# Optimization experiments

Hardware: AMD Instinct MI355X
Metric: run time of the kernel (lower is better)

## Reference

```python
import jax, jax.numpy as jnp
import numpy as np

N, NF, INF, NHID = 8192, 128, 128, 16


def _gcn(x, adj, dis, W, b):
    # GraphConvolution: support = x @ W; aggregate with distance-weighted adjacency
    support = x @ W  # [N, out]
    return (adj * dis) @ support + b


def setup_inputs() -> dict:
    key = jax.random.key(0)
    ks = jax.random.split(key, 26)

    def lin(k, i, o):
        kw, kb = jax.random.split(k)
        W = jax.random.uniform(kw, (i, o), jnp.float32, -1.0, 1.0) / np.sqrt(i).astype(np.float32)
        b = jax.random.uniform(kb, (o,), jnp.float32, -1.0, 1.0) / np.sqrt(i).astype(np.float32)
        return W, b

    x = jax.random.normal(ks[0], (N, NF), jnp.float32)
    adj = jax.random.uniform(ks[1], (N, N), jnp.float32)
    dis = jax.random.uniform(ks[2], (N, N), jnp.float32)

    W1, b1 = lin(ks[3], NF, NF)        # linear1
    Wg1, bg1 = lin(ks[4], NF, INF)     # gc1
    Wm1, bm1 = lin(ks[5], INF, 64)     # linear_med1
    Wm2, bm2 = lin(ks[6], 64, 128)     # linear_med2
    Wm3, bm3 = lin(ks[7], 128, 64)     # linear_med3
    Wm4, bm4 = lin(ks[8], 64, 64)      # linear_med4
    Wgh, bgh = lin(ks[9], 64, 64)      # gconv_hidden[0]
    W2, b2 = lin(ks[10], 64, 32)       # linear2
    Wg2, bg2 = lin(ks[11], 32, 32)     # gc2
    W3, b3 = lin(ks[12], 32, NHID)     # linear3

    return dict(x=x, adj=adj, dis=dis, W1=W1, b1=b1, Wg1=Wg1, bg1=bg1,
                Wm1=Wm1, bm1=bm1, Wm2=Wm2, bm2=bm2, Wm3=Wm3, bm3=bm3,
                Wm4=Wm4, bm4=bm4, Wgh=Wgh, bgh=bgh, W2=W2, b2=b2,
                Wg2=Wg2, bg2=bg2, W3=W3, b3=b3)


def reference(x, adj, dis, W1, b1, Wg1, bg1, Wm1, bm1, Wm2, bm2, Wm3, bm3,
              Wm4, bm4, Wgh, bgh, W2, b2, Wg2, bg2, W3, b3):
    lrelu = lambda v: jax.nn.leaky_relu(v, 0.2)
    x0 = _gcn(x @ W1 + b1, adj, dis, Wg1, bg1)
    x0 = lrelu(x0 @ Wm1 + bm1)
    x0 = lrelu(x0 @ Wm2 + bm2)
    x0 = lrelu(x0 @ Wm3 + bm3)
    x0 = jax.nn.relu(x0 @ Wm4 + bm4)
    x_res = x0
    x0 = jax.nn.relu(_gcn(x0, adj, dis, Wgh, bgh) + x_res)  # one hidden gconv layer
    x0 = x0 @ W2 + b2
    x0 = _gcn(x0, adj, dis, Wg2, bg2)
    return x0 @ W3 + b3
```

## Files before the change

### kernel.cpp

```cpp
#include <hip/hip_runtime.h>
#include <hip/hip_bf16.h>

#define NROWS 8192
typedef unsigned short u16;
typedef short bf16x8 __attribute__((ext_vector_type(8)));
typedef short bf16x4 __attribute__((ext_vector_type(4)));
typedef float f32x4 __attribute__((ext_vector_type(4)));

__device__ __forceinline__ u16 f2b(float f) {
    unsigned u = __float_as_uint(f);
    unsigned r = (u + 0x7fffu + ((u >> 16) & 1u)) >> 16;
    return (u16)r;
}
__device__ __forceinline__ float b2f(u16 v) {
    return __uint_as_float(((unsigned)v) << 16);
}

template<int MODE> __device__ __forceinline__ float actf(float v) {
    if constexpr (MODE == 1) return fmaxf(v, 0.f);
    else if constexpr (MODE == 2) return v > 0.f ? v : 0.2f * v;
    else return v;
}

__global__ __launch_bounds__(256) void fold1(
    const float* __restrict__ W1, const float* __restrict__ b1,
    const float* __restrict__ Wg1,
    const float* __restrict__ W2, const float* __restrict__ b2,
    const float* __restrict__ Wg2, float* __restrict__ ws) {
    float* T2 = ws + 9376;
    float* v1 = ws + 11424;
    float* v2 = ws + 11552;
    float* T1 = ws + 16384;
    const int tid = threadIdx.x, b = blockIdx.x;
    if (b < 16) {
        int i = b * 8 + (tid >> 5), j4 = (tid & 31) << 2;
        float4 acc = {0, 0, 0, 0};
        for (int k = 0; k < 128; ++k) {
            float a = W1[i * 128 + k];
            float4 g = *(const float4*)&Wg1[k * 128 + j4];
            acc.x += a * g.x; acc.y += a * g.y; acc.z += a * g.z; acc.w += a * g.w;
        }
        *(float4*)&T1[i * 128 + j4] = acc;
    } else if (b == 16) {
        if (tid < 128) {
            float s = 0;
            for (int k = 0; k < 128; ++k) s += b1[k] * Wg1[k * 128 + tid];
            v1[tid] = s;
        } else if (tid < 160) {
            int j = tid - 128;
            float s = 0;
            for (int k = 0; k < 32; ++k) s += b2[k] * Wg2[k * 32 + j];
            v2[j] = s;
        }
    } else {
        for (int o4 = tid; o4 < 64 * 8; o4 += 256) {
            int i = o4 >> 3, j4 = (o4 & 7) << 2;
            float4 acc = {0, 0, 0, 0};
            for (int k = 0; k < 32; ++k) {
                float a = W2[i * 32 + k];
                float4 g = *(const float4*)&Wg2[k * 32 + j4];
                acc.x += a * g.x; acc.y += a * g.y; acc.z += a * g.z; acc.w += a * g.w;
            }
            *(float4*)&T2[i * 32 + j4] = acc;
        }
    }
}

__global__ __launch_bounds__(256) void fold2(
    const float* __restrict__ Wm1, const float* __restrict__ bm1,
    const float* __restrict__ bg1,
    const float* __restrict__ W3, const float* __restrict__ b3,
    const float* __restrict__ bg2, float* __restrict__ ws) {
    float* WA = ws + 0;
    float* bA = ws + 8192;
    float* cA = ws + 8256;
    float* WB = ws + 8320;
    float* bB = ws + 9344;
    float* cB = ws + 9360;
    const float* T2 = ws + 9376;
    const float* v1 = ws + 11424;
    const float* v2 = ws + 11552;
    const float* T1 = ws + 16384;
    const int tid = threadIdx.x, b = blockIdx.x;
    if (b < 8) {
        int i = b * 16 + (tid >> 4), j4 = (tid & 15) << 2;
        float4 acc = {0, 0, 0, 0};
        for (int k = 0; k < 128; ++k) {
            float a = T1[i * 128 + k];
            float4 g = *(const float4*)&Wm1[k * 64 + j4];
            acc.x += a * g.x; acc.y += a * g.y; acc.z += a * g.z; acc.w += a * g.w;
        }
        *(float4*)&WA[i * 64 + j4] = acc;
    } else if (b == 8) {
        if (tid < 64) {
            float s = 0, c = 0;
            for (int k = 0; k < 128; ++k) {
                s += v1[k] * Wm1[k * 64 + tid];
                c += bg1[k] * Wm1[k * 64 + tid];
            }
            bA[tid] = s; cA[tid] = c + bm1[tid];
        } else if (tid < 80) {
            int j = tid - 64;
            float s = 0, c = 0;
            for (int k = 0; k < 32; ++k) {
                s += v2[k] * W3[k * 16 + j];
                c += bg2[k] * W3[k * 16 + j];
            }
            bB[j] = s; cB[j] = c + b3[j];
        }
    } else {
        int i = tid >> 2, j4 = (tid & 3) << 2;
        float4 acc = {0, 0, 0, 0};
        for (int k = 0; k < 32; ++k) {
            float a = T2[i * 32 + k];
            float4 g = *(const float4*)&W3[k * 16 + j4];
            acc.x += a * g.x; acc.y += a * g.y; acc.z += a * g.z; acc.w += a * g.w;
        }
        *(float4*)&WB[i * 16 + j4] = acc;
    }
}

template<int K, int M, int AIN, int AOUT, int OUTT>
__global__ __launch_bounds__(256) void gemm_rows(
    const float* __restrict__ in, const float* __restrict__ W,
    const float* __restrict__ bias, void* __restrict__ outv) {
    constexpr int RB = 32;
    constexpr int TNs = (M >= 64) ? 4 : 2;
    constexpr int TXs = M / TNs;
    constexpr int TYs = 256 / TXs;
    constexpr int TMs = RB / TYs;
    static_assert(TMs >= 1 && TMs * TYs == RB, "bad cfg");
    __shared__ float in_t[K][RB + 4];
    __shared__ float w_s[K * M];
    __shared__ float bias_s[M];
    const int tid = threadIdx.x;
    const int b0 = blockIdx.x * RB;
    constexpr int K4 = K / 4;
    for (int g = tid; g < RB * K4; g += 256) {
        int r = g / K4, c4 = g % K4;
        float4 v = *(const float4*)&in[(size_t)(b0 + r) * K + c4 * 4];
        v.x = actf<AIN>(v.x); v.y = actf<AIN>(v.y);
        v.z = actf<AIN>(v.z); v.w = actf<AIN>(v.w);
        in_t[c4 * 4 + 0][r] = v.x;
        in_t[c4 * 4 + 1][r] = v.y;
        in_t[c4 * 4 + 2][r] = v.z;
        in_t[c4 * 4 + 3][r] = v.w;
    }
    for (int g = tid; g < K * M / 4; g += 256)
        ((float4*)w_s)[g] = ((const float4*)W)[g];
    if (tid < M) bias_s[tid] = bias ? bias[tid] : 0.f;
    __syncthreads();

    const int tx = tid % TXs, ty = tid / TXs;
    const int c0 = tx * TNs, r0 = ty * TMs;
    float acc[TMs][TNs] = {};
    for (int k = 0; k < K; ++k) {
        float a[TMs];
#pragma unroll
        for (int m = 0; m < TMs; ++m) a[m] = in_t[k][r0 + m];
        float w[TNs];
#pragma unroll
        for (int n = 0; n < TNs; ++n) w[n] = w_s[k * M + c0 + n];
#pragma unroll
        for (int m = 0; m < TMs; ++m)
#pragma unroll
            for (int n = 0; n < TNs; ++n) acc[m][n] += a[m] * w[n];
    }
#pragma unroll
    for (int m = 0; m < TMs; ++m) {
        float vres[TNs];
#pragma unroll
        for (int n = 0; n < TNs; ++n) vres[n] = actf<AOUT>(acc[m][n] + bias_s[c0 + n]);
        if constexpr (OUTT == 0) {
            float* op = &((float*)outv)[(size_t)(b0 + r0 + m) * M + c0];
            if constexpr (TNs == 4) { float4 o4 = {vres[0], vres[1], vres[2], vres[3]}; *(float4*)op = o4; }
            else                    { float2 o2 = {vres[0], vres[1]}; *(float2*)op = o2; }
        } else {
            u16* ot = (u16*)outv;
#pragma unroll
            for (int n = 0; n < TNs; ++n)
                ot[(size_t)(c0 + n) * NROWS + (b0 + r0 + m)] = f2b(vres[n]);
        }
    }
}

template<int K, int M, int AOUT, int OMODE>
__device__ __forceinline__ void layer_step(
    const float (*pin)[17], const float* __restrict__ w,
    const float* __restrict__ bias,
    float (*pout)[17], float* __restrict__ gout, u16* __restrict__ stout,
    int b0, int tid) {
    constexpr int TXs = M / 4;
    constexpr int TYs = 256 / TXs;
    constexpr int TMs = 16 / TYs;
    static_assert(TMs >= 1, "cfg");
    const int tx = tid % TXs, ty = tid / TXs;
    const int c0 = tx * 4, r0 = ty * TMs;
    float acc[TMs][4] = {};
    for (int k = 0; k < K; ++k) {
        float4 wv = *(const float4*)&w[k * M + c0];
#pragma unroll
        for (int m = 0; m < TMs; ++m) {
            float a = pin[k][r0 + m];
            acc[m][0] += a * wv.x; acc[m][1] += a * wv.y;
            acc[m][2] += a * wv.z; acc[m][3] += a * wv.w;
        }
    }
#pragma unroll
    for (int m = 0; m < TMs; ++m) {
        float v[4];
#pragma unroll
        for (int n = 0; n < 4; ++n) {
            float bv = bias ? bias[c0 + n] : 0.f;
            v[n] = actf<AOUT>(acc[m][n] + bv);
        }
        if constexpr (OMODE != 2) {
#pragma unroll
            for (int n = 0; n < 4; ++n) pout[c0 + n][r0 + m] = v[n];
        }
        if constexpr (OMODE == 1) {
            float4 o = {v[0], v[1], v[2], v[3]};
            *(float4*)&gout[(size_t)(b0 + r0 + m) * M + c0] = o;
        }
        if constexpr (OMODE == 2) {
#pragma unroll
            for (int n = 0; n < 4; ++n)
                stout[(size_t)(c0 + n) * NROWS + (b0 + r0 + m)] = f2b(v[n]);
        }
    }
}

__global__ __launch_bounds__(256) void med_chain(
    const float* __restrict__ gA,
    const float* __restrict__ Wm2, const float* __restrict__ bm2,
    const float* __restrict__ Wm3, const float* __restrict__ bm3,
    const float* __restrict__ Wm4, const float* __restrict__ bm4,
    const float* __restrict__ Wgh,
    float* __restrict__ h4, u16* __restrict__ St) {
    __shared__ __align__(16) float P0[64][17];
    __shared__ __align__(16) float P1[128][17];
    __shared__ __align__(16) float P2[64][17];
    const int tid = threadIdx.x;
    const int b0 = blockIdx.x * 16;

    {
        int r = tid >> 4, c4 = tid & 15;
        float4 v = *(const float4*)&gA[(size_t)(b0 + r) * 64 + c4 * 4];
        P0[c4 * 4 + 0][r] = actf<2>(v.x);
        P0[c4 * 4 + 1][r] = actf<2>(v.y);
        P0[c4 * 4 + 2][r] = actf<2>(v.z);
        P0[c4 * 4 + 3][r] = actf<2>(v.w);
    }
    __syncthreads();
    layer_step<64, 128, 2, 0>(P0, Wm2, bm2, P1, nullptr, nullptr, b0, tid);
    __syncthreads();
    layer_step<128, 64, 2, 0>(P1, Wm3, bm3, P2, nullptr, nullptr, b0, tid);
    __syncthreads();
    layer_step<64, 64, 1, 1>(P2, Wm4, bm4, P0, h4, nullptr, b0, tid);
    __syncthreads();
    layer_step<64, 64, 0, 2>(P0, Wgh, nullptr, nullptr, nullptr, St, b0, tid);
}

template<int F, int MODE, int KS>
__global__ __launch_bounds__(256) void agg_mfma(
    u16* __restrict__ Abf, const float* __restrict__ adj,
    const float* __restrict__ dis, const u16* __restrict__ St,
    u16* __restrict__ Pout) {
    constexpr int CT = F / 16;
    constexpr int BK = 128;
    constexpr int KCH = NROWS / KS;
    constexpr int NCH = KCH / BK;
    __shared__ __align__(16) u16 As[64 * BK];
    __shared__ __align__(16) u16 Bs[F * BK];
    const int tid  = threadIdx.x;
    const int lane = tid & 63;
    const int wid  = tid >> 6;
    const int i0   = blockIdx.x * 64;
    const int ky   = blockIdx.y;
    const int l15  = lane & 15;
    const int kb   = (lane >> 4) * 8;
    const int k0   = ky * KCH;
    f32x4 acc[CT] = {};

    for (int ch = 0; ch < NCH; ++ch) {
        const int kc = k0 + ch * BK;
        if constexpr (MODE == 0) {
#pragma unroll
            for (int r = 0; r < (64 * BK) / (256 * 8); ++r) {
                int e8  = r * 256 + tid;
                int row = e8 >> 4;
                int col = (e8 & 15) * 8;
                bf16x8 v = *(const bf16x8*)(Abf + (size_t)(i0 + row) * NROWS + kc + col);
                int bo = ((row * BK + col) * 2) ^ ((row & 7) << 4);
                *(bf16x8*)((char*)As + bo) = v;
            }
        } else {
#pragma unroll
            for (int r = 0; r < (64 * BK) / (256 * 4); ++r) {
                int e4  = r * 256 + tid;
                int row = e4 >> 5;
                int col = (e4 & 31) * 4;
                size_t g = (size_t)(i0 + row) * NROWS + kc + col;
                f32x4 a = __builtin_nontemporal_load((const f32x4*)(adj + g));
                f32x4 d = __builtin_nontemporal_load((const f32x4*)(dis + g));
                bf16x4 v;
#pragma unroll
                for (int j = 0; j < 4; ++j) v[j] = (short)f2b(a[j] * d[j]);
                if constexpr (MODE == 1) *(bf16x4*)(Abf + g) = v;
                int bo = ((row * BK + col) * 2) ^ ((row & 7) << 4);
                *(bf16x4*)((char*)As + bo) = v;
            }
        }
#pragma unroll
        for (int r = 0; r < (F * BK) / (256 * 8); ++r) {
            int e8  = r * 256 + tid;
            int c   = e8 >> 4;
            int col = (e8 & 15) * 8;
            bf16x8 v = *(const bf16x8*)(St + (size_t)c * NROWS + kc + col);
            int bo = ((c * BK + col) * 2) ^ ((c & 7) << 4);
            *(bf16x8*)((char*)Bs + bo) = v;
        }
        __syncthreads();
#pragma unroll
        for (int ks = 0; ks < BK; ks += 32) {
            const int arow = wid * 16 + l15;
            int ao = ((arow * BK + ks + kb) * 2) ^ ((arow & 7) << 4);
            bf16x8 af = *(const bf16x8*)((const char*)As + ao);
#pragma unroll
            for (int ct = 0; ct < CT; ++ct) {
                int bcol = ct * 16 + l15;
                int bo = ((bcol * BK + ks + kb) * 2) ^ ((bcol & 7) << 4);
                bf16x8 bf = *(const bf16x8*)((const char*)Bs + bo);
                acc[ct] = __builtin_amdgcn_mfma_f32_16x16x32_bf16(af, bf, acc[ct], 0, 0, 0);
            }
        }
        __syncthreads();
    }
    u16* P = Pout + (size_t)ky * ((size_t)NROWS * F);
    const int rb = i0 + wid * 16 + (lane >> 4) * 4;
#pragma unroll
    for (int ct = 0; ct < CT; ++ct)
#pragma unroll
        for (int i = 0; i < 4; ++i)
            P[(size_t)(rb + i) * F + ct * 16 + l15] = f2b(acc[ct][i]);
}

template<int F, int KS>
__global__ __launch_bounds__(256) void reduce_add(
    const u16* __restrict__ P, const float* __restrict__ bias,
    const float* __restrict__ res, float* __restrict__ out) {
    constexpr int TOT8 = NROWS * F / 8;
    int i8 = blockIdx.x * 256 + threadIdx.x;
    if (i8 >= TOT8) return;
    constexpr size_t STR = (size_t)NROWS * F;
    float s[8] = {};
#pragma unroll
    for (int k = 0; k < KS; ++k) {
        bf16x8 v = *(const bf16x8*)(P + (size_t)k * STR + (size_t)i8 * 8);
#pragma unroll
        for (int j = 0; j < 8; ++j) s[j] += b2f((u16)v[j]);
    }
    const int c0 = (i8 * 8) % F;
#pragma unroll
    for (int j = 0; j < 8; ++j) s[j] += bias[c0 + j];
    if (res) {
        const float4* r4 = (const float4*)(res + (size_t)i8 * 8);
        float4 ra = r4[0], rb = r4[1];
        s[0] += ra.x; s[1] += ra.y; s[2] += ra.z; s[3] += ra.w;
        s[4] += rb.x; s[5] += rb.y; s[6] += rb.z; s[7] += rb.w;
    }
    float4* o4 = (float4*)(out + (size_t)i8 * 8);
    float4 oa = {s[0], s[1], s[2], s[3]}, ob = {s[4], s[5], s[6], s[7]};
    o4[0] = oa; o4[1] = ob;
}

extern "C" void kernel_launch(void* const* d_in, const int* in_sizes, int n_in,
                              void* d_out, int out_size, void* d_ws, size_t ws_size,
                              hipStream_t stream) {
    const float* x   = (const float*)d_in[0];
    const float* adj = (const float*)d_in[1];
    const float* dis = (const float*)d_in[2];
    const float* W1  = (const float*)d_in[3];
    const float* b1  = (const float*)d_in[4];
    const float* Wg1 = (const float*)d_in[5];
    const float* bg1 = (const float*)d_in[6];
    const float* Wm1 = (const float*)d_in[7];
    const float* bm1 = (const float*)d_in[8];
    const float* Wm2 = (const float*)d_in[9];
    const float* bm2 = (const float*)d_in[10];
    const float* Wm3 = (const float*)d_in[11];
    const float* bm3 = (const float*)d_in[12];
    const float* Wm4 = (const float*)d_in[13];
    const float* bm4 = (const float*)d_in[14];
    const float* Wgh = (const float*)d_in[15];
    const float* bgh = (const float*)d_in[16];
    const float* W2  = (const float*)d_in[17];
    const float* b2  = (const float*)d_in[18];
    const float* Wg2 = (const float*)d_in[19];
    const float* bg2 = (const float*)d_in[20];
    const float* W3  = (const float*)d_in[21];
    const float* b3  = (const float*)d_in[22];
    float* ws  = (float*)d_ws;
    float* out = (float*)d_out;

    constexpr int KS = 16;
    const size_t ABF_FLOATS = (size_t)NROWS * NROWS / 2;
    const size_t P_FLOATS = (size_t)KS * NROWS * 64 / 2;
    const size_t BASE_FLOATS = 40960 + 262144 + P_FLOATS + 524288 + 524288;
    const size_t NEED_PRE_BYTES = (ABF_FLOATS + BASE_FLOATS) * 4ULL;
    const bool pre = ws_size >= NEED_PRE_BYTES;

    float* base = ws + (pre ? ABF_FLOATS : 0);
    float* wsW  = base;
    float* St_f = wsW + 40960;
    float* P_f  = St_f + 262144;
    float* gA   = P_f + P_FLOATS;
    float* h4   = gA + 524288;
    float* g2   = gA;

    u16* Abf = (u16*)ws;
    u16* St  = (u16*)St_f;
    u16* P   = (u16*)P_f;
    const float* WA = wsW + 0;
    const float* bA = wsW + 8192;
    const float* cA = wsW + 8256;
    const float* WB = wsW + 8320;
    const float* bB = wsW + 9344;
    const float* cB = wsW + 9360;

    fold1<<<18, 256, 0, stream>>>(W1, b1, Wg1, W2, b2, Wg2, wsW);
    fold2<<<10, 256, 0, stream>>>(Wm1, bm1, bg1, W3, b3, bg2, wsW);

    gemm_rows<128, 64, 0, 0, 1><<<256, 256, 0, stream>>>(x, WA, bA, St);
    if (pre) agg_mfma<64, 1, KS><<<dim3(128, KS), 256, 0, stream>>>(Abf, adj, dis, St, P);
    else     agg_mfma<64, 2, KS><<<dim3(128, KS), 256, 0, stream>>>(nullptr, adj, dis, St, P);
    reduce_add<64, KS><<<256, 256, 0, stream>>>(P, cA, nullptr, gA);

    med_chain<<<512, 256, 0, stream>>>(gA, Wm2, bm2, Wm3, bm3, Wm4, bm4, Wgh, h4, St);

    if (pre) agg_mfma<64, 0, KS><<<dim3(128, KS), 256, 0, stream>>>(Abf, nullptr, nullptr, St, P);
    else     agg_mfma<64, 2, KS><<<dim3(128, KS), 256, 0, stream>>>(nullptr, adj, dis, St, P);
    reduce_add<64, KS><<<256, 256, 0, stream>>>(P, bgh, h4, g2);

    gemm_rows<64, 16, 1, 0, 1><<<256, 256, 0, stream>>>(g2, WB, bB, St);
    if (pre) agg_mfma<16, 0, KS><<<dim3(128, KS), 256, 0, stream>>>(Abf, nullptr, nullptr, St, P);
    else     agg_mfma<16, 2, KS><<<dim3(128, KS), 256, 0, stream>>>(nullptr, adj, dis, St, P);
    reduce_add<16, KS><<<64, 256, 0, stream>>>(P, cB, nullptr, out);
}
```

Before: 326.0 us.

## Prefetch next A/B tiles into registers during MFMA and halve split-K

The aggregation kernel now loads the next K chunk of the adjacency/distance (or cached bf16 adjacency) tile and the support tile into registers while the MFMAs for the current chunk run, then writes them to shared memory after a barrier. This is meant to hide global-memory latency behind compute in a bandwidth-bound kernel. The split-K factor also drops from 16 to 8, which halves the partial-sum buffer and the reduction traffic but leaves fewer blocks in the grid. The register prefetch raises VGPR pressure, notably in the fp32 adj/dis mode, which may lower occupancy.

After: 312.8 us. -4.0%, faster.

```diff
diff --git a/kernel.cpp b/kernel.cpp
--- a/kernel.cpp
+++ b/kernel.cpp
@@ -261,6 +261,53 @@
     layer_step<64, 64, 0, 2>(P0, Wgh, nullptr, nullptr, nullptr, St, b0, tid);
 }
 
+#define LOAD_A(KC) \
+    if constexpr (MODE == 0) { \
+        _Pragma("unroll") for (int r = 0; r < AR8; ++r) { \
+            int e8 = r * 256 + tid; \
+            rA[r] = *(const bf16x8*)(Abf + (size_t)(i0 + (e8 >> 4)) * NROWS + (KC) + (e8 & 15) * 8); \
+        } \
+    } else { \
+        _Pragma("unroll") for (int r = 0; r < AR4; ++r) { \
+            int e4 = r * 256 + tid; \
+            size_t g = (size_t)(i0 + (e4 >> 5)) * NROWS + (KC) + (e4 & 31) * 4; \
+            rAa[r] = __builtin_nontemporal_load((const f32x4*)(adj + g)); \
+            rAd[r] = __builtin_nontemporal_load((const f32x4*)(dis + g)); \
+        } \
+    }
+
+#define LOAD_B(KC) \
+    _Pragma("unroll") for (int r = 0; r < BR8; ++r) { \
+        int e8 = r * 256 + tid; \
+        rB[r] = *(const bf16x8*)(St + (size_t)(e8 >> 4) * NROWS + (KC) + (e8 & 15) * 8); \
+    }
+
+#define STORE_A(KC) \
+    if constexpr (MODE == 0) { \
+        _Pragma("unroll") for (int r = 0; r < AR8; ++r) { \
+            int e8 = r * 256 + tid; int row = e8 >> 4; int col = (e8 & 15) * 8; \
+            int bo = ((row * BK + col) * 2) ^ ((row & 7) << 4); \
+            *(bf16x8*)((char*)As + bo) = rA[r]; \
+        } \
+    } else { \
+        _Pragma("unroll") for (int r = 0; r < AR4; ++r) { \
+            int e4 = r * 256 + tid; int row = e4 >> 5; int col = (e4 & 31) * 4; \
+            bf16x4 v; \
+            _Pragma("unroll") for (int j = 0; j < 4; ++j) v[j] = (short)f2b(rAa[r][j] * rAd[r][j]); \
+            if constexpr (MODE == 1) \
+                *(bf16x4*)(Abf + (size_t)(i0 + row) * NROWS + (KC) + col) = v; \
+            int bo = ((row * BK + col) * 2) ^ ((row & 7) << 4); \
+            *(bf16x4*)((char*)As + bo) = v; \
+        } \
+    }
+
+#define STORE_B() \
+    _Pragma("unroll") for (int r = 0; r < BR8; ++r) { \
+        int e8 = r * 256 + tid; int c = e8 >> 4; int col = (e8 & 15) * 8; \
+        int bo = ((c * BK + col) * 2) ^ ((c & 7) << 4); \
+        *(bf16x8*)((char*)Bs + bo) = rB[r]; \
+    }
+
 template<int F, int MODE, int KS>
 __global__ __launch_bounds__(256) void agg_mfma(
     u16* __restrict__ Abf, const float* __restrict__ adj,
@@ -270,6 +317,9 @@
     constexpr int BK = 128;
     constexpr int KCH = NROWS / KS;
     constexpr int NCH = KCH / BK;
+    constexpr int AR8 = (64 * BK) / (256 * 8);
+    constexpr int AR4 = (64 * BK) / (256 * 4);
+    constexpr int BR8 = (F * BK) / (256 * 8);
     __shared__ __align__(16) u16 As[64 * BK];
     __shared__ __align__(16) u16 Bs[F * BK];
     const int tid  = threadIdx.x;
@@ -281,46 +331,22 @@
     const int kb   = (lane >> 4) * 8;
     const int k0   = ky * KCH;
     f32x4 acc[CT] = {};
-
+    bf16x8 rA[AR8];
+    f32x4 rAa[AR4], rAd[AR4];
+    bf16x8 rB[BR8];
+
+    LOAD_A(k0)
+    LOAD_B(k0)
     for (int ch = 0; ch < NCH; ++ch) {
         const int kc = k0 + ch * BK;
-        if constexpr (MODE == 0) {
-#pragma unroll
-            for (int r = 0; r < (64 * BK) / (256 * 8); ++r) {
-                int e8  = r * 256 + tid;
-                int row = e8 >> 4;
-                int col = (e8 & 15) * 8;
-                bf16x8 v = *(const bf16x8*)(Abf + (size_t)(i0 + row) * NROWS + kc + col);
-                int bo = ((row * BK + col) * 2) ^ ((row & 7) << 4);
-                *(bf16x8*)((char*)As + bo) = v;
-            }
-        } else {
-#pragma unroll
-            for (int r = 0; r < (64 * BK) / (256 * 4); ++r) {
-                int e4  = r * 256 + tid;
-                int row = e4 >> 5;
-                int col = (e4 & 31) * 4;
-                size_t g = (size_t)(i0 + row) * NROWS + kc + col;
-                f32x4 a = __builtin_nontemporal_load((const f32x4*)(adj + g));
-                f32x4 d = __builtin_nontemporal_load((const f32x4*)(dis + g));
-                bf16x4 v;
-#pragma unroll
-                for (int j = 0; j < 4; ++j) v[j] = (short)f2b(a[j] * d[j]);
-                if constexpr (MODE == 1) *(bf16x4*)(Abf + g) = v;
-                int bo = ((row * BK + col) * 2) ^ ((row & 7) << 4);
-                *(bf16x4*)((char*)As + bo) = v;
-            }
-        }
-#pragma unroll
-        for (int r = 0; r < (F * BK) / (256 * 8); ++r) {
-            int e8  = r * 256 + tid;
-            int c   = e8 >> 4;
-            int col = (e8 & 15) * 8;
-            bf16x8 v = *(const bf16x8*)(St + (size_t)c * NROWS + kc + col);
-            int bo = ((c * BK + col) * 2) ^ ((c & 7) << 4);
-            *(bf16x8*)((char*)Bs + bo) = v;
-        }
         __syncthreads();
+        STORE_A(kc)
+        STORE_B()
+        __syncthreads();
+        if (ch + 1 < NCH) {
+            LOAD_A(kc + BK)
+            LOAD_B(kc + BK)
+        }
 #pragma unroll
         for (int ks = 0; ks < BK; ks += 32) {
             const int arow = wid * 16 + l15;
@@ -334,7 +360,6 @@
                 acc[ct] = __builtin_amdgcn_mfma_f32_16x16x32_bf16(af, bf, acc[ct], 0, 0, 0);
             }
         }
-        __syncthreads();
     }
     u16* P = Pout + (size_t)ky * ((size_t)NROWS * F);
     const int rb = i0 + wid * 16 + (lane >> 4) * 4;
@@ -344,6 +369,10 @@
         for (int i = 0; i < 4; ++i)
             P[(size_t)(rb + i) * F + ct * 16 + l15] = f2b(acc[ct][i]);
 }
+#undef LOAD_A
+#undef LOAD_B
+#undef STORE_A
+#undef STORE_B
 
 template<int F, int KS>
 __global__ __launch_bounds__(256) void reduce_add(
@@ -403,7 +432,7 @@
     float* ws  = (float*)d_ws;
     float* out = (float*)d_out;
 
-    constexpr int KS = 16;
+    constexpr int KS = 8;
     const size_t ABF_FLOATS = (size_t)NROWS * NROWS / 2;
     const size_t P_FLOATS = (size_t)KS * NROWS * 64 / 2;
     const size_t BASE_FLOATS = 40960 + 262144 + P_FLOATS + 524288 + 524288;
```
